# Kernel optimization log

Measured on AMD Instinct MI355X. Metric: run time of the kernel, lower is better.

## Reference

```python
import jax, jax.numpy as jnp
import numpy as np
import math

HEAD_DIM = 64
N_Q = 64
N_KV = 8
HIDDEN = 2880
SLIDING = 128
BASE = 150000.0
INIT_CTX = 4096
SCALE = 32.0
NTK_A = 1.0
NTK_B = 32.0
SEQ = 2048


def _rope_cos_sin(position_ids):
    # YaRN-scaled inverse frequencies (scaling_factor > 1 branch)
    freq = BASE ** (jnp.arange(0, HEAD_DIM, 2, dtype=jnp.float32) / HEAD_DIM)
    concentration = 0.1 * math.log(SCALE) + 1.0
    d_half = HEAD_DIM // 2
    low = d_half * math.log(INIT_CTX / (NTK_B * 2 * math.pi)) / math.log(BASE)
    high = d_half * math.log(INIT_CTX / (NTK_A * 2 * math.pi)) / math.log(BASE)
    interpolation = 1.0 / (SCALE * freq)
    extrapolation = 1.0 / freq
    ramp = (jnp.arange(d_half, dtype=jnp.float32) - low) / (high - low)
    mask = 1.0 - jnp.clip(ramp, 0.0, 1.0)
    inv_freq = interpolation * (1.0 - mask) + extrapolation * mask
    freqs = position_ids.astype(jnp.float32)[:, None] * inv_freq[None, :]  # [n, d/2]
    return jnp.cos(freqs) * concentration, jnp.sin(freqs) * concentration


def _apply_rope(x, cos, sin):
    # x: [n, h, d]; cos/sin: [n, d/2]
    cos = cos[:, None, :].astype(x.dtype)
    sin = sin[:, None, :].astype(x.dtype)
    x1, x2 = jnp.split(x, 2, axis=-1)
    return jnp.concatenate([x1 * cos - x2 * sin, x2 * cos + x1 * sin], axis=-1)


def setup_inputs() -> dict:
    key = jax.random.key(0)
    ks = jax.random.split(key, 6)
    qkv_dim = HEAD_DIM * (N_Q + 2 * N_KV)
    return {
        "hidden_states": jax.random.normal(ks[0], (SEQ, HIDDEN), dtype=jnp.float32),
        "qkv_w": jax.random.normal(ks[1], (qkv_dim, HIDDEN), dtype=jnp.float32) * 0.02,
        "qkv_b": jax.random.normal(ks[2], (qkv_dim,), dtype=jnp.float32) * 0.02,
        "o_w": jax.random.normal(ks[3], (HIDDEN, N_Q * HEAD_DIM), dtype=jnp.float32) * 0.02,
        "o_b": jax.random.normal(ks[4], (HIDDEN,), dtype=jnp.float32) * 0.02,
        "sinks": jax.random.normal(ks[5], (N_Q,), dtype=jnp.float32),
        "position_ids": jnp.arange(SEQ, dtype=jnp.int64 if jax.config.jax_enable_x64 else jnp.int32),
    }


def reference(hidden_states, qkv_w, qkv_b, o_w, o_b, sinks, position_ids):
    n = hidden_states.shape[0]
    scaling = HEAD_DIM ** (-0.5)

    # fused QKV projection + split
    qkv = hidden_states @ qkv_w.T + qkv_b  # [n, (nq+2*nkv)*d]
    q_sz, k_sz = N_Q * HEAD_DIM, N_KV * HEAD_DIM
    q = qkv[:, :q_sz].reshape(n, N_Q, HEAD_DIM)
    k = qkv[:, q_sz:q_sz + k_sz].reshape(n, N_KV, HEAD_DIM)
    v = qkv[:, q_sz + k_sz:].reshape(n, N_KV, HEAD_DIM)

    # RoPE (YaRN)
    cos, sin = _rope_cos_sin(position_ids)
    q = _apply_rope(q, cos, sin)
    k = _apply_rope(k, cos, sin)

    # GQA: repeat KV heads to match query heads
    groups = N_Q // N_KV
    k_full = jnp.repeat(k, groups, axis=1)  # [n, N_Q, d]
    v_full = jnp.repeat(v, groups, axis=1)

    scores = jnp.einsum('qhd,khd->hqk', q, k_full) * scaling  # [H, S, S]

    # sliding-window mask (distance > window -> -inf), as in source (no causal term)
    current_pos = position_ids.max()
    key_pos = current_pos - n + 1 + jnp.arange(n)
    dist = position_ids[:, None] - key_pos[None, :]
    win_mask = jnp.where(dist > SLIDING, -jnp.inf, 0.0).astype(scores.dtype)
    scores = scores + win_mask[None, :, :]

    # learned sink logit appended to softmax normalization
    sink = jnp.broadcast_to(sinks[:, None, None], (N_Q, n, 1)).astype(scores.dtype)
    logits = jnp.concatenate([scores, sink], axis=-1)  # [H, S, S+1]
    probs = jax.nn.softmax(logits, axis=-1)[..., :-1]   # drop sink column

    attn = jnp.einsum('hqk,khd->qhd', probs, v_full)    # [S, H, d]
    attn = attn.reshape(n, N_Q * HEAD_DIM)
    return attn @ o_w.T + o_b
```

## Files before the change

### kernel.cpp

```cpp
#include <hip/hip_runtime.h>
#include <hip/hip_bf16.h>
#include <stdint.h>

typedef __attribute__((ext_vector_type(4))) float f32x4;
typedef __attribute__((ext_vector_type(8))) short bf16x8;

#define SEQ 2048
#define HIDDEN 2880
#define NQ 64
#define NKV 8
#define HD 64
#define QKV_DIM 5120
#define Q_SZ 4096
#define K_SZ 512
#define OW_N 2880
#define OW_NPAD 2944
#define OW_K 4096

__device__ __forceinline__ unsigned short f2b_bits(float f) {
    unsigned int x = __float_as_uint(f);
    unsigned int r = (x + 0x7fffu + ((x >> 16) & 1u)) >> 16;
    return (unsigned short)r;
}
__device__ __forceinline__ float b2f(unsigned short u) {
    return __uint_as_float(((unsigned int)u) << 16);
}

__device__ __forceinline__ void llds16(const ushort* g, ushort* l) {
    __builtin_amdgcn_global_load_lds(
        (const __attribute__((address_space(1))) void*)g,
        (__attribute__((address_space(3))) void*)l, 16, 0, 0);
}

__global__ void convert_f32(const float* __restrict__ in, ushort* __restrict__ out, int n4) {
    int i = blockIdx.x * blockDim.x + threadIdx.x;
    int stride = gridDim.x * blockDim.x;
    for (; i < n4; i += stride) {
        float4 v = reinterpret_cast<const float4*>(in)[i];
        ushort4 o = make_ushort4(f2b_bits(v.x), f2b_bits(v.y), f2b_bits(v.z), f2b_bits(v.w));
        reinterpret_cast<ushort4*>(out)[i] = o;
    }
}

__global__ void convert_ow(const float* __restrict__ in, ushort* __restrict__ out) {
    int i = blockIdx.x * blockDim.x + threadIdx.x;
    const int n4 = OW_NPAD * OW_K / 4;
    int stride = gridDim.x * blockDim.x;
    for (; i < n4; i += stride) {
        int row = (i * 4) >> 12;
        ushort4 o;
        if (row < OW_N) {
            float4 v = reinterpret_cast<const float4*>(in)[i];
            o = make_ushort4(f2b_bits(v.x), f2b_bits(v.y), f2b_bits(v.z), f2b_bits(v.w));
        } else {
            o = make_ushort4(0, 0, 0, 0);
        }
        reinterpret_cast<ushort4*>(out)[i] = o;
    }
}

template<int OUT_BF16>
__global__ __launch_bounds__(256) void gemm_bt(
    const ushort* __restrict__ A, const ushort* __restrict__ B,
    const float* __restrict__ bias, void* __restrict__ Cout,
    int M, int N, int K, int Nreal, int ldC)
{
    __shared__ __align__(16) ushort As[128 * 64];
    __shared__ __align__(16) ushort Bs[128 * 64];
    const int tid = threadIdx.x;
    const int lane = tid & 63;
    const int w = tid >> 6;
    const int wr = w >> 1, wc = w & 1;
    const int m0 = blockIdx.y * 128, n0 = blockIdx.x * 128;

    f32x4 acc[4][4] = {};

    for (int k0 = 0; k0 < K; k0 += 64) {
        #pragma unroll
        for (int it = 0; it < 4; ++it) {
            int i = it * 256 + tid;
            int row = i >> 3;
            int col16 = (i ^ (row & 7)) & 7;
            const ushort* ga = A + (size_t)(m0 + row) * K + k0 + col16 * 8;
            ushort* la = As + (size_t)(it * 256 + (tid & ~63)) * 8;
            llds16(ga, la);
            const ushort* gb = B + (size_t)(n0 + row) * K + k0 + col16 * 8;
            ushort* lb = Bs + (size_t)(it * 256 + (tid & ~63)) * 8;
            llds16(gb, lb);
        }
        __syncthreads();
        #pragma unroll
        for (int kk = 0; kk < 2; ++kk) {
            bf16x8 a[4], b[4];
            #pragma unroll
            for (int mi = 0; mi < 4; ++mi) {
                int row = wr * 64 + mi * 16 + (lane & 15);
                int byte = row * 128 + kk * 64 + (lane >> 4) * 16;
                byte ^= (row & 7) << 4;
                a[mi] = *reinterpret_cast<const bf16x8*>(reinterpret_cast<const char*>(As) + byte);
            }
            #pragma unroll
            for (int ni = 0; ni < 4; ++ni) {
                int row = wc * 64 + ni * 16 + (lane & 15);
                int byte = row * 128 + kk * 64 + (lane >> 4) * 16;
                byte ^= (row & 7) << 4;
                b[ni] = *reinterpret_cast<const bf16x8*>(reinterpret_cast<const char*>(Bs) + byte);
            }
            #pragma unroll
            for (int mi = 0; mi < 4; ++mi)
                #pragma unroll
                for (int ni = 0; ni < 4; ++ni)
                    acc[mi][ni] = __builtin_amdgcn_mfma_f32_16x16x32_bf16(a[mi], b[ni], acc[mi][ni], 0, 0, 0);
        }
        __syncthreads();
    }

    #pragma unroll
    for (int mi = 0; mi < 4; ++mi) {
        int gr = m0 + wr * 64 + mi * 16 + (lane >> 4) * 4;
        #pragma unroll
        for (int ni = 0; ni < 4; ++ni) {
            int gc = n0 + wc * 64 + ni * 16 + (lane & 15);
            if (gc < Nreal) {
                float bv = bias[gc];
                #pragma unroll
                for (int r = 0; r < 4; ++r) {
                    float v = acc[mi][ni][r] + bv;
                    if (OUT_BF16)
                        ((ushort*)Cout)[(size_t)(gr + r) * ldC + gc] = f2b_bits(v);
                    else
                        ((float*)Cout)[(size_t)(gr + r) * ldC + gc] = v;
                }
            }
        }
    }
}

__global__ __launch_bounds__(256) void rope_kernel(
    const ushort* __restrict__ qkv, const int* __restrict__ pos,
    ushort* __restrict__ q_ro, ushort* __restrict__ k_ro)
{
    __shared__ float cosv[32], sinv[32];
    const int s = blockIdx.x;
    const int tid = threadIdx.x;
    if (tid < 32) {
        int j = tid;
        const float logbase = logf(150000.0f);
        float freq = expf((float)j * (logbase / 32.0f));
        float interp = 1.0f / (32.0f * freq);
        float extrap = 1.0f / freq;
        const float twopi = 6.283185307179586f;
        float low  = 32.0f * logf(4096.0f / (32.0f * twopi)) / logbase;
        float high = 32.0f * logf(4096.0f / (1.0f  * twopi)) / logbase;
        float ramp = ((float)j - low) / (high - low);
        float mask = 1.0f - fminf(fmaxf(ramp, 0.0f), 1.0f);
        float inv_freq = interp * (1.0f - mask) + extrap * mask;
        float ang = (float)pos[s] * inv_freq;
        const float conc = 0.1f * logf(32.0f) + 1.0f;
        cosv[j] = cosf(ang) * conc;
        sinv[j] = sinf(ang) * conc;
    }
    __syncthreads();
    const float qsc = 0.125f * 1.4426950408889634f;
    #pragma unroll
    for (int it = 0; it < 8; ++it) {
        int idx = it * 256 + tid;
        int h = idx >> 5, j = idx & 31;
        const ushort* src = qkv + (size_t)s * QKV_DIM + h * HD;
        float x1 = b2f(src[j]), x2 = b2f(src[j + 32]);
        float c = cosv[j], sn = sinv[j];
        ushort* dst = q_ro + ((size_t)h * SEQ + s) * HD;
        dst[j]      = f2b_bits((x1 * c - x2 * sn) * qsc);
        dst[j + 32] = f2b_bits((x2 * c + x1 * sn) * qsc);
    }
    {
        int h = tid >> 5, j = tid & 31;
        const ushort* src = qkv + (size_t)s * QKV_DIM + Q_SZ + h * HD;
        float x1 = b2f(src[j]), x2 = b2f(src[j + 32]);
        float c = cosv[j], sn = sinv[j];
        ushort* dst = k_ro + ((size_t)h * SEQ + s) * HD;
        dst[j]      = f2b_bits(x1 * c - x2 * sn);
        dst[j + 32] = f2b_bits(x2 * c + x1 * sn);
    }
}

__global__ __launch_bounds__(256) void vtrans_kernel(const ushort* __restrict__ qkv, ushort* __restrict__ vT) {
    __shared__ ushort t[64][65];
    const int kh = blockIdx.x >> 5;
    const int s0 = (blockIdx.x & 31) * 64;
    const int tid = threadIdx.x;
    #pragma unroll
    for (int it = 0; it < 16; ++it) {
        int e = it * 256 + tid;
        int sl = e >> 6, d = e & 63;
        t[d][sl] = qkv[(size_t)(s0 + sl) * QKV_DIM + Q_SZ + K_SZ + kh * HD + d];
    }
    __syncthreads();
    #pragma unroll
    for (int it = 0; it < 16; ++it) {
        int e = it * 256 + tid;
        int d = e >> 6, sl = e & 63;
        vT[((size_t)kh * HD + d) * SEQ + s0 + sl] = t[d][sl];
    }
}

__global__ __launch_bounds__(256, 5) void attn_kernel(
    const ushort* __restrict__ q_ro, const ushort* __restrict__ k_ro,
    const ushort* __restrict__ vT, const float* __restrict__ sinks,
    ushort* __restrict__ attn_out)
{
    __shared__ __align__(16) ushort Kb[2][4096];
    __shared__ __align__(16) ushort Vb[4096];
    __shared__ __align__(16) ushort Pl[4][1024];

    const int tid = threadIdx.x;
    const int lane = tid & 63;
    const int w = tid >> 6;
    const int l15 = lane & 15;
    const int l4 = lane >> 4;

    int wg = blockIdx.x;
    int wgid = (wg & 7) * 128 + (wg >> 3);
    const int kh = wgid >> 7;
    const int qh = (wgid >> 4) & 7;
    const int pp = wgid & 15;
    const int h = kh * 8 + qh;

    const float snk = sinks[h];
    char* pbase = (char*)&Pl[w][0];

    const short oneb = (short)0x3F80;
    const bf16x8 bones = {oneb, oneb, oneb, oneb, oneb, oneb, oneb, oneb};

    auto stageK = [&](int bs, int k0) {
        #pragma unroll
        for (int it = 0; it < 2; ++it) {
            int i = it * 256 + tid;
            int r = i >> 3;
            int cs = (i & 7) ^ (r & 7);
            llds16(k_ro + ((size_t)(kh * SEQ + k0 + r)) * 64 + cs * 8,
                   &Kb[bs][(it * 256 + (tid & ~63)) * 8]);
        }
    };
    auto stageV = [&](int k0) {
        #pragma unroll
        for (int it = 0; it < 2; ++it) {
            int i = it * 256 + tid;
            int r = i >> 3;
            int cs = (i & 7) ^ (r & 7);
            llds16(vT + ((size_t)(kh * 64 + r)) * SEQ + k0 + cs * 8,
                   &Vb[(it * 256 + (tid & ~63)) * 8]);
        }
    };

    for (int sidx = 0; sidx < 2; ++sidx) {
        const int qt = sidx ? (31 - pp) : pp;
        const int q0 = qt * 64;
        const int qw = q0 + w * 16;

        bf16x8 aq[2];
        #pragma unroll
        for (int kc = 0; kc < 2; ++kc)
            aq[kc] = *reinterpret_cast<const bf16x8*>(
                q_ro + ((size_t)h * SEQ + qw + l15) * HD + kc * 32 + l4 * 8);

        f32x4 o[4] = {};
        f32x4 lacc = {0.f, 0.f, 0.f, 0.f};

        const int kt0 = (qt >= 2) ? (qt - 2) : 0;
        int cur = 0;

        stageK(0, kt0 * 64);
        __syncthreads();

        auto tile_body = [&](int kt, bool pref) {
            const int k0 = kt * 64;
            stageV(k0);
            if (pref) stageK(cur ^ 1, k0 + 64);

            f32x4 s[4];
            const f32x4 z = {0.f, 0.f, 0.f, 0.f};
            __builtin_amdgcn_s_setprio(1);
            #pragma unroll
            for (int c = 0; c < 4; ++c) {
                int rowK = c * 16 + l15;
                int byt0 = rowK * 128 + l4 * 16;
                byt0 ^= (rowK & 7) << 4;
                bf16x8 bk0 = *reinterpret_cast<const bf16x8*>((const char*)Kb[cur] + byt0);
                s[c] = __builtin_amdgcn_mfma_f32_16x16x32_bf16(aq[0], bk0, z, 0, 0, 0);
                bf16x8 bk1 = *reinterpret_cast<const bf16x8*>((const char*)Kb[cur] + (byt0 ^ 64));
                s[c] = __builtin_amdgcn_mfma_f32_16x16x32_bf16(aq[1], bk1, s[c], 0, 0, 0);
            }
            __builtin_amdgcn_s_setprio(0);

            if (k0 < qw - 113) {
                #pragma unroll
                for (int c = 0; c < 4; ++c) {
                    int kg = k0 + c * 16 + l15;
                    #pragma unroll
                    for (int r = 0; r < 4; ++r) {
                        int qg = qw + l4 * 4 + r;
                        if (qg - kg > 128) s[c][r] = -1e30f;
                    }
                }
            }

            #pragma unroll
            for (int c = 0; c < 4; ++c)
                #pragma unroll
                for (int r = 0; r < 4; ++r) {
                    float pv = exp2f(s[c][r]);
                    int row = l4 * 4 + r;
                    int byte = row * 128 + (c * 16 + l15) * 2;
                    byte ^= (row & 7) << 4;
                    *reinterpret_cast<ushort*>(pbase + byte) = f2b_bits(pv);
                }

            if (pref) asm volatile("s_waitcnt vmcnt(2)\n\ts_barrier" ::: "memory");
            else      asm volatile("s_waitcnt vmcnt(0)\n\ts_barrier" ::: "memory");

            __builtin_amdgcn_s_setprio(1);
            #pragma unroll
            for (int kc = 0; kc < 2; ++kc) {
                int byteP = l15 * 128 + kc * 64 + l4 * 16;
                byteP ^= (l15 & 7) << 4;
                bf16x8 pa = *reinterpret_cast<const bf16x8*>(pbase + byteP);
                lacc = __builtin_amdgcn_mfma_f32_16x16x32_bf16(pa, bones, lacc, 0, 0, 0);
                #pragma unroll
                for (int df = 0; df < 4; ++df) {
                    int rowV = df * 16 + l15;
                    int byte = rowV * 128 + kc * 64 + l4 * 16;
                    byte ^= (rowV & 7) << 4;
                    bf16x8 bv = *reinterpret_cast<const bf16x8*>((const char*)Vb + byte);
                    o[df] = __builtin_amdgcn_mfma_f32_16x16x32_bf16(pa, bv, o[df], 0, 0, 0);
                }
            }
            __builtin_amdgcn_s_setprio(0);

            __syncthreads();
            cur ^= 1;
        };

        for (int kt = kt0; kt < SEQ / 64 - 1; ++kt) tile_body(kt, true);
        tile_body(SEQ / 64 - 1, false);

        {
            const float es = exp2f(snk * 1.4426950408889634f);
            float inv[4];
            #pragma unroll
            for (int r = 0; r < 4; ++r) inv[r] = 1.0f / (lacc[r] + es);
            #pragma unroll
            for (int df = 0; df < 4; ++df)
                #pragma unroll
                for (int r = 0; r < 4; ++r) {
                    int row = qw + l4 * 4 + r;
                    int col = df * 16 + l15;
                    attn_out[(size_t)row * Q_SZ + h * HD + col] = f2b_bits(o[df][r] * inv[r]);
                }
        }
    }
}

extern "C" void kernel_launch(void* const* d_in, const int* in_sizes, int n_in,
                              void* d_out, int out_size, void* d_ws, size_t ws_size,
                              hipStream_t stream) {
    const float* hidden = (const float*)d_in[0];
    const float* qkv_w  = (const float*)d_in[1];
    const float* qkv_b  = (const float*)d_in[2];
    const float* o_w    = (const float*)d_in[3];
    const float* o_b    = (const float*)d_in[4];
    const float* sinks  = (const float*)d_in[5];
    const int*   pos    = (const int*)d_in[6];
    float* out = (float*)d_out;

    char* ws = (char*)d_ws;
    size_t off = 0;
    auto alloc = [&](size_t bytes) {
        char* p = ws + off;
        off += (bytes + 255) & ~(size_t)255;
        return p;
    };
    ushort* hs_bf   = (ushort*)alloc((size_t)SEQ * HIDDEN * 2);
    ushort* wqkv_bf = (ushort*)alloc((size_t)QKV_DIM * HIDDEN * 2);
    ushort* qkv_bf  = (ushort*)alloc((size_t)SEQ * QKV_DIM * 2);
    ushort* q_ro    = (ushort*)alloc((size_t)NQ * SEQ * HD * 2);
    ushort* k_ro    = (ushort*)alloc((size_t)NKV * SEQ * HD * 2);
    ushort* vT      = (ushort*)alloc((size_t)NKV * HD * SEQ * 2);
    ushort* attn_bf = (ushort*)alloc((size_t)SEQ * Q_SZ * 2);
    ushort* wo_bf   = (ushort*)alloc((size_t)OW_NPAD * OW_K * 2);

    convert_f32<<<2048, 256, 0, stream>>>(hidden, hs_bf, SEQ * HIDDEN / 4);
    convert_f32<<<2048, 256, 0, stream>>>(qkv_w, wqkv_bf, QKV_DIM * HIDDEN / 4);
    convert_ow<<<2048, 256, 0, stream>>>(o_w, wo_bf);

    gemm_bt<1><<<dim3(QKV_DIM / 128, SEQ / 128), 256, 0, stream>>>(
        hs_bf, wqkv_bf, qkv_b, qkv_bf, SEQ, QKV_DIM, HIDDEN, QKV_DIM, QKV_DIM);

    rope_kernel<<<SEQ, 256, 0, stream>>>(qkv_bf, pos, q_ro, k_ro);
    vtrans_kernel<<<NKV * 32, 256, 0, stream>>>(qkv_bf, vT);

    attn_kernel<<<1024, 256, 0, stream>>>(q_ro, k_ro, vT, sinks, attn_bf);

    gemm_bt<0><<<dim3(OW_NPAD / 128, SEQ / 128), 256, 0, stream>>>(
        attn_bf, wo_bf, o_b, out, SEQ, OW_NPAD, OW_K, OW_N, OW_N);
}
```

Before: 289.6 us.

## Double-buffer V with K, transpose score MFMA for packed bf16 P writes

V tiles are now double-buffered and prefetched one tile ahead together with K through a single precomputed-address stage routine. This removes the mid-tile vmcnt wait plus barrier, since each wave's P buffer is private and only the end-of-tile sync remains. The QK^T MFMA operands are swapped so each lane holds four consecutive keys of one query row. That lets P be packed with v_cvt_pk_bf16_f32 and written as 8-byte stores, and it simplifies the sliding-window mask to one threshold compare. The price is more LDS and launch bounds lowered from 5 to 4 waves, which can reduce occupancy; there is also a redundant dead P load and a reliance on the end barrier to cover the async LDS loads.

```diff
diff --git a/kernel.cpp b/kernel.cpp
--- a/kernel.cpp
+++ b/kernel.cpp
@@ -204,13 +204,13 @@
     }
 }
 
-__global__ __launch_bounds__(256, 5) void attn_kernel(
+__global__ __launch_bounds__(256, 4) void attn_kernel(
     const ushort* __restrict__ q_ro, const ushort* __restrict__ k_ro,
     const ushort* __restrict__ vT, const float* __restrict__ sinks,
     ushort* __restrict__ attn_out)
 {
     __shared__ __align__(16) ushort Kb[2][4096];
-    __shared__ __align__(16) ushort Vb[4096];
+    __shared__ __align__(16) ushort Vb[2][4096];
     __shared__ __align__(16) ushort Pl[4][1024];
 
     const int tid = threadIdx.x;
@@ -232,25 +232,24 @@
     const short oneb = (short)0x3F80;
     const bf16x8 bones = {oneb, oneb, oneb, oneb, oneb, oneb, oneb, oneb};
 
-    auto stageK = [&](int bs, int k0) {
-        #pragma unroll
-        for (int it = 0; it < 2; ++it) {
-            int i = it * 256 + tid;
-            int r = i >> 3;
-            int cs = (i & 7) ^ (r & 7);
-            llds16(k_ro + ((size_t)(kh * SEQ + k0 + r)) * 64 + cs * 8,
-                   &Kb[bs][(it * 256 + (tid & ~63)) * 8]);
-        }
-    };
-    auto stageV = [&](int k0) {
-        #pragma unroll
-        for (int it = 0; it < 2; ++it) {
-            int i = it * 256 + tid;
-            int r = i >> 3;
-            int cs = (i & 7) ^ (r & 7);
-            llds16(vT + ((size_t)(kh * 64 + r)) * SEQ + k0 + cs * 8,
-                   &Vb[(it * 256 + (tid & ~63)) * 8]);
-        }
+    const int i0 = tid, i1 = 256 + tid;
+    const int r0 = i0 >> 3, cs0 = (i0 ^ r0) & 7;
+    const int r1 = i1 >> 3, cs1 = (i1 ^ r1) & 7;
+    const ushort* gK0 = k_ro + (size_t)kh * (SEQ * 64) + r0 * 64 + cs0 * 8;
+    const ushort* gK1 = k_ro + (size_t)kh * (SEQ * 64) + r1 * 64 + cs1 * 8;
+    const ushort* gV0 = vT + ((size_t)kh * 64 + r0) * SEQ + cs0 * 8;
+    const ushort* gV1 = vT + ((size_t)kh * 64 + r1) * SEQ + cs1 * 8;
+    const int ld0 = (tid & ~63) * 8, ld1 = (256 + (tid & ~63)) * 8;
+
+    const int swz = (l15 & 7) << 4;
+    const int kvbase = l15 * 128 + ((l4 * 16) ^ swz);
+    const int pwbase = l15 * 128 + ((l4 * 8) ^ swz);
+
+    auto stage = [&](int bs, int k0) {
+        llds16(gK0 + k0 * 64, &Kb[bs][ld0]);
+        llds16(gK1 + k0 * 64, &Kb[bs][ld1]);
+        llds16(gV0 + k0,      &Vb[bs][ld0]);
+        llds16(gV1 + k0,      &Vb[bs][ld1]);
     };
 
     for (int sidx = 0; sidx < 2; ++sidx) {
@@ -270,68 +269,56 @@
         const int kt0 = (qt >= 2) ? (qt - 2) : 0;
         int cur = 0;
 
-        stageK(0, kt0 * 64);
+        stage(0, kt0 * 64);
         __syncthreads();
 
-        auto tile_body = [&](int kt, bool pref) {
+        for (int kt = kt0; kt < SEQ / 64; ++kt) {
             const int k0 = kt * 64;
-            stageV(k0);
-            if (pref) stageK(cur ^ 1, k0 + 64);
+            if (kt + 1 < SEQ / 64) stage(cur ^ 1, k0 + 64);
 
             f32x4 s[4];
             const f32x4 z = {0.f, 0.f, 0.f, 0.f};
+            const char* kbp = (const char*)Kb[cur];
             __builtin_amdgcn_s_setprio(1);
             #pragma unroll
             for (int c = 0; c < 4; ++c) {
-                int rowK = c * 16 + l15;
-                int byt0 = rowK * 128 + l4 * 16;
-                byt0 ^= (rowK & 7) << 4;
-                bf16x8 bk0 = *reinterpret_cast<const bf16x8*>((const char*)Kb[cur] + byt0);
-                s[c] = __builtin_amdgcn_mfma_f32_16x16x32_bf16(aq[0], bk0, z, 0, 0, 0);
-                bf16x8 bk1 = *reinterpret_cast<const bf16x8*>((const char*)Kb[cur] + (byt0 ^ 64));
-                s[c] = __builtin_amdgcn_mfma_f32_16x16x32_bf16(aq[1], bk1, s[c], 0, 0, 0);
+                bf16x8 bk0 = *reinterpret_cast<const bf16x8*>(kbp + c * 2048 + kvbase);
+                s[c] = __builtin_amdgcn_mfma_f32_16x16x32_bf16(bk0, aq[0], z, 0, 0, 0);
+                bf16x8 bk1 = *reinterpret_cast<const bf16x8*>(kbp + c * 2048 + (kvbase ^ 64));
+                s[c] = __builtin_amdgcn_mfma_f32_16x16x32_bf16(bk1, aq[1], s[c], 0, 0, 0);
             }
             __builtin_amdgcn_s_setprio(0);
 
             if (k0 < qw - 113) {
-                #pragma unroll
-                for (int c = 0; c < 4; ++c) {
-                    int kg = k0 + c * 16 + l15;
+                int thr = qw + l15 - 128 - k0;
+                #pragma unroll
+                for (int c = 0; c < 4; ++c)
                     #pragma unroll
-                    for (int r = 0; r < 4; ++r) {
-                        int qg = qw + l4 * 4 + r;
-                        if (qg - kg > 128) s[c][r] = -1e30f;
-                    }
-                }
-            }
-
-            #pragma unroll
-            for (int c = 0; c < 4; ++c)
-                #pragma unroll
-                for (int r = 0; r < 4; ++r) {
-                    float pv = exp2f(s[c][r]);
-                    int row = l4 * 4 + r;
-                    int byte = row * 128 + (c * 16 + l15) * 2;
-                    byte ^= (row & 7) << 4;
-                    *reinterpret_cast<ushort*>(pbase + byte) = f2b_bits(pv);
-                }
-
-            if (pref) asm volatile("s_waitcnt vmcnt(2)\n\ts_barrier" ::: "memory");
-            else      asm volatile("s_waitcnt vmcnt(0)\n\ts_barrier" ::: "memory");
-
+                    for (int r = 0; r < 4; ++r)
+                        if (c * 16 + l4 * 4 + r < thr) s[c][r] = -1e30f;
+            }
+
+            #pragma unroll
+            for (int c = 0; c < 4; ++c) {
+                float p0 = exp2f(s[c][0]), p1 = exp2f(s[c][1]);
+                float p2 = exp2f(s[c][2]), p3 = exp2f(s[c][3]);
+                unsigned int pk0, pk1;
+                asm("v_cvt_pk_bf16_f32 %0, %1, %2" : "=v"(pk0) : "v"(p0), "v"(p1));
+                asm("v_cvt_pk_bf16_f32 %0, %1, %2" : "=v"(pk1) : "v"(p2), "v"(p3));
+                uint2 pv; pv.x = pk0; pv.y = pk1;
+                *reinterpret_cast<uint2*>(pbase + (pwbase ^ (c * 32))) = pv;
+            }
+
+            const char* vbp = (const char*)Vb[cur];
             __builtin_amdgcn_s_setprio(1);
             #pragma unroll
             for (int kc = 0; kc < 2; ++kc) {
-                int byteP = l15 * 128 + kc * 64 + l4 * 16;
-                byteP ^= (l15 & 7) << 4;
-                bf16x8 pa = *reinterpret_cast<const bf16x8*>(pbase + byteP);
+                bf16x8 pa = *reinterpret_cast<const bf16x8*>(pbase + (kvbase ^ (kc * 64)) - (kvbase & ~2047) + (l15 * 128 + ((l4 * 16) ^ swz) - l15 * 128));
+                pa = *reinterpret_cast<const bf16x8*>(pbase + ((l15 * 128 + ((l4 * 16) ^ swz)) ^ (kc * 64)));
                 lacc = __builtin_amdgcn_mfma_f32_16x16x32_bf16(pa, bones, lacc, 0, 0, 0);
                 #pragma unroll
                 for (int df = 0; df < 4; ++df) {
-                    int rowV = df * 16 + l15;
-                    int byte = rowV * 128 + kc * 64 + l4 * 16;
-                    byte ^= (rowV & 7) << 4;
-                    bf16x8 bv = *reinterpret_cast<const bf16x8*>((const char*)Vb + byte);
+                    bf16x8 bv = *reinterpret_cast<const bf16x8*>(vbp + df * 2048 + (kvbase ^ (kc * 64)));
                     o[df] = __builtin_amdgcn_mfma_f32_16x16x32_bf16(pa, bv, o[df], 0, 0, 0);
                 }
             }
@@ -339,10 +326,7 @@
 
             __syncthreads();
             cur ^= 1;
-        };
-
-        for (int kt = kt0; kt < SEQ / 64 - 1; ++kt) tile_body(kt, true);
-        tile_body(SEQ / 64 - 1, false);
+        }
 
         {
             const float es = exp2f(snk * 1.4426950408889634f);
```

Measured after the change: 275.2 us. 5.0% less time.
